# Kernel optimization log

Measured on AMD Instinct MI355X. Metric: run time of the kernel, lower is better.

The kernel has to match this reference:

```python
import jax, jax.numpy as jnp
import numpy as np

EPS_LN = 1e-5
EPS_ATTN = 1e-8
NUM_ITER = 3

B, N, DIN = 64, 4096, 256
K, D, H = 8, 256, 512


def layer_norm(x, g, b):
    m = jnp.mean(x, axis=-1, keepdims=True)
    v = jnp.mean((x - m) ** 2, axis=-1, keepdims=True)
    return (x - m) * jax.lax.rsqrt(v + EPS_LN) * g + b


def gru_cell(x, h, W_ih, b_ih, W_hh, b_hh):
    # torch GRUCell: gates ordered (reset, update, new)
    gi = x @ W_ih.T + b_ih  # [BK, 3D]
    gh = h @ W_hh.T + b_hh
    ir, iz, inn = jnp.split(gi, 3, axis=-1)
    hr, hz, hn = jnp.split(gh, 3, axis=-1)
    r = jax.nn.sigmoid(ir + hr)
    z = jax.nn.sigmoid(iz + hz)
    n = jnp.tanh(inn + r * hn)
    return (1.0 - z) * n + z * h


def setup_inputs() -> dict:
    key = jax.random.key(0)
    ks = jax.random.split(key, 16)
    s = 1.0 / np.sqrt(D)
    si = 1.0 / np.sqrt(DIN)
    inp = {
        'inputs': jax.random.normal(ks[0], (B, N, DIN), jnp.float32),
        'noise': jax.random.normal(ks[1], (B, K, D), jnp.float32),
        'slot_mu': jax.random.normal(ks[2], (1, 1, D), jnp.float32),
        'slot_log_sigma': jnp.zeros((1, 1, D), jnp.float32),
        'Wq': jax.random.uniform(ks[3], (D, D), jnp.float32, -s, s),
        'bq': jnp.zeros((D,), jnp.float32),
        'Wk': jax.random.uniform(ks[4], (D, DIN), jnp.float32, -si, si),
        'bk': jnp.zeros((D,), jnp.float32),
        'Wv': jax.random.uniform(ks[5], (D, DIN), jnp.float32, -si, si),
        'bv': jnp.zeros((D,), jnp.float32),
        'W_ih': jax.random.uniform(ks[6], (3 * D, D), jnp.float32, -s, s),
        'b_ih': jnp.zeros((3 * D,), jnp.float32),
        'W_hh': jax.random.uniform(ks[7], (3 * D, D), jnp.float32, -s, s),
        'b_hh': jnp.zeros((3 * D,), jnp.float32),
        'ln_in_g': jnp.ones((DIN,), jnp.float32), 'ln_in_b': jnp.zeros((DIN,), jnp.float32),
        'ln_s_g': jnp.ones((D,), jnp.float32), 'ln_s_b': jnp.zeros((D,), jnp.float32),
        'ln_ff_g': jnp.ones((D,), jnp.float32), 'ln_ff_b': jnp.zeros((D,), jnp.float32),
        'W1': jax.random.uniform(ks[8], (H, D), jnp.float32, -s, s),
        'b1': jnp.zeros((H,), jnp.float32),
        'W2': jax.random.uniform(ks[9], (D, H), jnp.float32, -1.0 / np.sqrt(H), 1.0 / np.sqrt(H)),
        'b2': jnp.zeros((D,), jnp.float32),
    }
    return inp


def reference(inputs, noise, slot_mu, slot_log_sigma, Wq, bq, Wk, bk, Wv, bv,
              W_ih, b_ih, W_hh, b_hh, ln_in_g, ln_in_b, ln_s_g, ln_s_b,
              ln_ff_g, ln_ff_b, W1, b1, W2, b2):
    scale = D ** -0.5
    slots = slot_mu + jnp.exp(slot_log_sigma) * noise  # [B,K,D]
    x = layer_norm(inputs, ln_in_g, ln_in_b)
    k = x @ Wk.T + bk  # [B,N,D]
    v = x @ Wv.T + bv  # [B,N,D]
    attn = None
    for _ in range(NUM_ITER):
        slots_prev = slots
        sn = layer_norm(slots, ln_s_g, ln_s_b)
        q = sn @ Wq.T + bq  # [B,K,D]
        dots = jnp.einsum('bkd,bnd->bkn', q, k) * scale
        attn = jax.nn.softmax(dots, axis=1)  # softmax over slots
        attn_norm = attn / (jnp.sum(attn, axis=-1, keepdims=True) + EPS_ATTN)
        updates = jnp.einsum('bkn,bnd->bkd', attn_norm, v)
        h = gru_cell(updates.reshape(-1, D), slots_prev.reshape(-1, D),
                     W_ih, b_ih, W_hh, b_hh).reshape(slots.shape)
        ff = layer_norm(h, ln_ff_g, ln_ff_b)
        slots = h + (jax.nn.relu(ff @ W1.T + b1) @ W2.T + b2)
    return slots, attn
```

## Files before the change

### kernel.cpp

```cpp
#include <hip/hip_runtime.h>
#include <hip/hip_bf16.h>
#include <math.h>

typedef __bf16 bf16x8 __attribute__((ext_vector_type(8)));
typedef float f32x4 __attribute__((ext_vector_type(4)));

#define DEV static __device__ __forceinline__

DEV unsigned short f2b(float f){
  unsigned int u = __float_as_uint(f);
  u += 0x7fffu + ((u>>16)&1u);
  return (unsigned short)(u>>16);
}
DEV float b2f(unsigned short h){ return __uint_as_float(((unsigned int)h)<<16); }
DEV unsigned int pck(float a, float b){
  return (unsigned int)f2b(a) | ((unsigned int)f2b(b)<<16);
}
DEV f32x4 mfma16(bf16x8 a, bf16x8 b, f32x4 c){
  return __builtin_amdgcn_mfma_f32_16x16x32_bf16(a,b,c,0,0,0);
}
DEV float sigm(float x){ return 1.f/(1.f+expf(-x)); }

__global__ __launch_bounds__(256) void k_slots_init(
    const float* __restrict__ noise, const float* __restrict__ mu,
    const float* __restrict__ ls, float* __restrict__ sf,
    unsigned short* __restrict__ sb){
  int i = blockIdx.x*256 + threadIdx.x;
  int d = i & 255;
  float val = mu[d] + expf(ls[d]) * noise[i];
  sf[i] = val; sb[i] = f2b(val);
}

__global__ __launch_bounds__(256) void k_prep_b16(
    const float* __restrict__ Whh, const float* __restrict__ W1,
    const float* __restrict__ W2,
    unsigned short* __restrict__ Whhb, unsigned short* __restrict__ W1b,
    unsigned short* __restrict__ W2b){
  int i = blockIdx.x*256 + threadIdx.x;
  if (i < 196608) Whhb[i] = f2b(Whh[i]);
  else if (i < 327680) W1b[i-196608] = f2b(W1[i-196608]);
  else if (i < 458752) W2b[i-327680] = f2b(W2[i-327680]);
}

__global__ __launch_bounds__(256) void k_pre1(
    const float* __restrict__ Wq, const float* __restrict__ Wk,
    const float* __restrict__ bq, const float* __restrict__ bk,
    unsigned short* __restrict__ WcT, float* __restrict__ bc,
    float* __restrict__ wqbk, float* __restrict__ cbk){
  int c = blockIdx.x, d = threadIdx.x;
  float acc = 0.f;
  for (int e=0;e<256;e++)
    acc += Wq[e*256+d] * Wk[e*256+c];
  WcT[c*256+d] = f2b(acc);
  __shared__ float red[256];
  red[d] = bq[d] * Wk[d*256+c];
  __syncthreads();
  for (int s2=128;s2>0;s2>>=1){ if (d<s2) red[d]+=red[d+s2]; __syncthreads(); }
  if (d==0) bc[c] = red[0];
  if (blockIdx.x==0){
    float a2=0.f;
    for (int e=0;e<256;e++) a2 += Wq[e*256+d]*bk[e];
    wqbk[d] = a2;
    __syncthreads();
    red[d] = bq[d]*bk[d];
    __syncthreads();
    for (int s2=128;s2>0;s2>>=1){ if (d<s2) red[d]+=red[d+s2]; __syncthreads(); }
    if (d==0) cbk[0] = red[0];
  }
}

__global__ __launch_bounds__(256) void k_pre2(
    const float* __restrict__ W_ih, const float* __restrict__ Wv,
    const float* __restrict__ bv, const float* __restrict__ b_ih,
    unsigned short* __restrict__ WvihT, float* __restrict__ bvih){
  int j = blockIdx.x, c = threadIdx.x;
  float acc=0.f;
  for (int d=0; d<256; d++)
    acc += W_ih[j*256+d] * Wv[d*256+c];
  WvihT[j*256+c] = f2b(acc);
  __shared__ float red[256];
  red[c] = bv[c] * W_ih[j*256+c];
  __syncthreads();
  for (int s2=128;s2>0;s2>>=1){ if (c<s2) red[c]+=red[c+s2]; __syncthreads(); }
  if (c==0) bvih[j] = red[0] + b_ih[j];
}

__global__ __launch_bounds__(256) void k_slot_q(
    const float* __restrict__ sf, const float* __restrict__ g,
    const float* __restrict__ be,
    const unsigned short* __restrict__ WcT, const float* __restrict__ bc,
    const float* __restrict__ wqbk, const float* __restrict__ cbk,
    unsigned short* __restrict__ qp, float* __restrict__ dotbias,
    float* __restrict__ attn_sum){
  __shared__ __align__(16) unsigned short sn[16][264];
  int b = blockIdx.x, t = threadIdx.x;
  if (t < 8) attn_sum[b*8+t] = 0.f;
  if (t < 8) dotbias[b*16+8+t] = 0.f;
  int r = t>>5, j = t&31;
  const float* pr = sf + (b*8+r)*256 + j*8;
  float v[8]; float s=0.f;
  #pragma unroll
  for (int i=0;i<8;i++){ v[i]=pr[i]; s+=v[i]; }
  s += __shfl_xor(s,1); s+=__shfl_xor(s,2); s+=__shfl_xor(s,4);
  s += __shfl_xor(s,8); s+=__shfl_xor(s,16);
  float m = s*(1.f/256.f);
  float vs=0.f;
  #pragma unroll
  for (int i=0;i<8;i++){ float d = v[i]-m; vs += d*d; }
  vs += __shfl_xor(vs,1); vs+=__shfl_xor(vs,2); vs+=__shfl_xor(vs,4);
  vs += __shfl_xor(vs,8); vs+=__shfl_xor(vs,16);
  float rstd = rsqrtf(vs*(1.f/256.f) + 1e-5f);
  float dp = 0.f;
  #pragma unroll
  for (int i=0;i<8;i++){
    int d = j*8+i;
    float snv = (v[i]-m)*rstd*g[d] + be[d];
    sn[r][d] = f2b(snv);
    dp += snv * wqbk[d];
  }
  dp += __shfl_xor(dp,1); dp+=__shfl_xor(dp,2); dp+=__shfl_xor(dp,4);
  dp += __shfl_xor(dp,8); dp+=__shfl_xor(dp,16);
  if (j==0) dotbias[b*16+r] = dp + cbk[0];
  for (int rr=8; rr<16; ++rr){ sn[rr][t]=0; if (t<8) sn[rr][256+t]=0; }
  __syncthreads();
  int lane = t&63, wv = t>>6, l16 = lane&15, quad = lane>>4;
  #pragma unroll
  for (int nt=0; nt<4; ++nt){
    int col = (wv*4+nt)*16 + l16;
    f32x4 acc = {0.f,0.f,0.f,0.f};
    #pragma unroll
    for (int kk=0;kk<8;kk++){
      int kd = kk*32 + quad*8;
      bf16x8 a = *(const bf16x8*)&sn[l16][kd];
      bf16x8 bb = *(const bf16x8*)(WcT + col*256 + kd);
      acc = mfma16(a,bb,acc);
    }
    float bcv = bc[col];
    #pragma unroll
    for (int ri=0;ri<4;ri++){
      int rw = quad*4+ri;
      qp[(b*16+rw)*256 + col] = f2b(acc[ri] + bcv);
    }
  }
}

__global__ __launch_bounds__(256) void k_iter(
    const float* __restrict__ in, const float* __restrict__ g,
    const float* __restrict__ be, const unsigned short* __restrict__ qp,
    const float* __restrict__ dotbias, float* __restrict__ attn_sum,
    float* __restrict__ upart, float* __restrict__ attn_out,
    const unsigned short* __restrict__ xc_r, unsigned short* __restrict__ xc_w){
  __shared__ __align__(16) unsigned short xt[64][264];
  __shared__ __align__(16) float al[64][8];
  __shared__ float bsum[8];
  int t = threadIdx.x;
  int b = blockIdx.x >> 3, sp = blockIdx.x & 7;
  if (t<8) bsum[t]=0.f;
  int lane=t&63, wv=t>>6, l16=lane&15, quad=lane>>4;
  bf16x8 aq[8];
  #pragma unroll
  for (int kk=0;kk<8;kk++)
    aq[kk] = *(const bf16x8*)(qp + ((size_t)(b*16+l16))*256 + kk*32+quad*8);
  float db[4];
  #pragma unroll
  for (int ri=0;ri<4;ri++) db[ri] = dotbias[b*16 + quad*4 + ri];
  float acc8[8] = {0.f,0.f,0.f,0.f,0.f,0.f,0.f,0.f};
  int rl = t>>3, j = t&7;
  for (int tile=0; tile<8; ++tile){
    int n0 = sp*512 + tile*64;
    __syncthreads();
    if (xc_r){
      #pragma unroll
      for (int p=0;p<2;p++){
        int row = p*32 + rl;
        const unsigned short* pr = xc_r + ((size_t)(b*4096 + n0 + row))*256 + j*32;
        #pragma unroll
        for (int c=0;c<4;c++)
          *(uint4*)&xt[row][j*32 + c*8] = *(const uint4*)(pr + c*8);
      }
    } else {
      #pragma unroll
      for (int p=0;p<2;p++){
        int row = p*32 + rl;
        const float* pr = in + ((size_t)(b*4096 + n0 + row))*256 + j*32;
        float v[32]; float s=0.f;
        #pragma unroll
        for (int c=0;c<8;c++) *(float4*)(v+c*4) = *(const float4*)(pr + c*4);
        #pragma unroll
        for (int i=0;i<32;i++) s += v[i];
        s += __shfl_xor(s,1); s+=__shfl_xor(s,2); s+=__shfl_xor(s,4);
        float m = s*(1.f/256.f);
        float vs=0.f;
        #pragma unroll
        for (int i=0;i<32;i++){ float d=v[i]-m; vs+=d*d; }
        vs+=__shfl_xor(vs,1); vs+=__shfl_xor(vs,2); vs+=__shfl_xor(vs,4);
        float rstd = rsqrtf(vs*(1.f/256.f)+1e-5f);
        #pragma unroll
        for (int c=0;c<4;c++){
          float o[8];
          #pragma unroll
          for (int q=0;q<8;q++){
            int d = j*32 + c*8 + q;
            o[q] = (v[c*8+q]-m)*rstd*g[d] + be[d];
          }
          uint4 w4;
          w4.x=pck(o[0],o[1]); w4.y=pck(o[2],o[3]);
          w4.z=pck(o[4],o[5]); w4.w=pck(o[6],o[7]);
          *(uint4*)&xt[row][j*32 + c*8] = w4;
          if (xc_w)
            *(uint4*)(xc_w + ((size_t)(b*4096 + n0 + row))*256 + j*32 + c*8) = w4;
        }
      }
    }
    __syncthreads();
    f32x4 acc = {0.f,0.f,0.f,0.f};
    #pragma unroll
    for (int kk=0;kk<8;kk++){
      int kd = kk*32 + quad*8;
      bf16x8 bb = *(const bf16x8*)&xt[wv*16 + l16][kd];
      acc = mfma16(aq[kk],bb,acc);
    }
    const float scale = 0.0625f;
    float val[4];
    #pragma unroll
    for (int ri=0;ri<4;ri++) val[ri] = (acc[ri] + db[ri]) * scale;
    float mx = fmaxf(fmaxf(val[0],val[1]), fmaxf(val[2],val[3]));
    mx = fmaxf(mx, __shfl_xor(mx,16));
    float e[4], s4=0.f;
    #pragma unroll
    for (int ri=0;ri<4;ri++){ e[ri] = expf(val[ri]-mx); s4 += e[ri]; }
    float s8 = s4 + __shfl_xor(s4,16);
    float inv = 1.f/s8;
    if (quad < 2){
      int nl = wv*16 + l16;
      #pragma unroll
      for (int ri=0;ri<4;ri++){
        float av = e[ri]*inv;
        int kr = quad*4+ri;
        al[nl][kr] = av;
        if (attn_out)
          attn_out[((size_t)(b*8+kr))*4096 + n0 + nl] = av;
        float ss = av;
        ss += __shfl_xor(ss,1); ss+=__shfl_xor(ss,2);
        ss += __shfl_xor(ss,4); ss+=__shfl_xor(ss,8);
        if (l16==0) atomicAdd(&bsum[kr], ss);
      }
    }
    __syncthreads();
    int c = t;
    for (int n=0;n<64;++n){
      float xv = b2f(xt[n][c]);
      float4 a0 = *(const float4*)&al[n][0];
      float4 a1 = *(const float4*)&al[n][4];
      acc8[0]+=a0.x*xv; acc8[1]+=a0.y*xv; acc8[2]+=a0.z*xv; acc8[3]+=a0.w*xv;
      acc8[4]+=a1.x*xv; acc8[5]+=a1.y*xv; acc8[6]+=a1.z*xv; acc8[7]+=a1.w*xv;
    }
  }
  float* o = upart + (size_t)sp*131072 + ((size_t)b*8)*256 + t;
  #pragma unroll
  for (int k2=0;k2<8;k2++) o[(size_t)k2*256] = acc8[k2];
  if (t<8) atomicAdd(&attn_sum[b*8+t], bsum[t]);
}

__global__ __launch_bounds__(256) void k_step(
    const float* __restrict__ upart, float* __restrict__ asum,
    float* __restrict__ sf, unsigned short* __restrict__ sb,
    const unsigned short* __restrict__ WvihT, const float* __restrict__ bvih,
    const unsigned short* __restrict__ Whhb, const float* __restrict__ bhh,
    const float* __restrict__ lnffg, const float* __restrict__ lnffb,
    const unsigned short* __restrict__ W1b, const float* __restrict__ b1,
    const unsigned short* __restrict__ W2b, const float* __restrict__ b2v,
    const float* __restrict__ lnsg, const float* __restrict__ lnsb,
    const unsigned short* __restrict__ WcT, const float* __restrict__ bc,
    const float* __restrict__ wqbk, const float* __restrict__ cbk,
    unsigned short* __restrict__ qp, float* __restrict__ dotb,
    float* __restrict__ out_slots, int last){
  __shared__ __align__(16) unsigned short ub16[16][264];
  __shared__ __align__(16) float hls[16][268];
  __shared__ __align__(16) unsigned short sn[16][264];
  __shared__ __align__(16) unsigned short s1t[16][520];
  __shared__ float redh[4][16], redq[4][16], mr[16], rs[16];
  int t = threadIdx.x;
  int Bk = blockIdx.x;
  int bb0 = Bk*2;
  int lane=t&63, wv=t>>6, l16=lane&15, quad=lane>>4;
  {
    int r16 = t>>4, c0 = (t&15)*16;
    size_t base = ((size_t)(Bk*16 + r16))*256 + c0;
    float4 a0={0,0,0,0}, a1={0,0,0,0}, a2={0,0,0,0}, a3={0,0,0,0};
    #pragma unroll
    for (int sp2=0; sp2<8; ++sp2){
      const float* p = upart + (size_t)sp2*131072 + base;
      float4 u0=*(const float4*)(p+0), u1=*(const float4*)(p+4),
             u2=*(const float4*)(p+8), u3=*(const float4*)(p+12);
      a0.x+=u0.x;a0.y+=u0.y;a0.z+=u0.z;a0.w+=u0.w;
      a1.x+=u1.x;a1.y+=u1.y;a1.z+=u1.z;a1.w+=u1.w;
      a2.x+=u2.x;a2.y+=u2.y;a2.z+=u2.z;a2.w+=u2.w;
      a3.x+=u3.x;a3.y+=u3.y;a3.z+=u3.z;a3.w+=u3.w;
    }
    float inv = 1.f/(asum[Bk*16 + r16] + 1e-8f);
    float uu[16] = {a0.x,a0.y,a0.z,a0.w,a1.x,a1.y,a1.z,a1.w,
                    a2.x,a2.y,a2.z,a2.w,a3.x,a3.y,a3.z,a3.w};
    #pragma unroll
    for (int c=0;c<16;c+=2){
      *(unsigned int*)&ub16[r16][c0+c] = pck(uu[c]*inv, uu[c+1]*inv);
    }
  }
  __syncthreads();
  if (t < 16) asum[Bk*16 + t] = 0.f;
  bf16x8 afi[8], afh[8];
  #pragma unroll
  for (int kk=0;kk<8;kk++){
    int kd = kk*32+quad*8;
    afi[kk] = *(const bf16x8*)&ub16[l16][kd];
    afh[kk] = *(const bf16x8*)(sb + ((size_t)(Bk*16+l16))*256 + kd);
  }
  float sh[4]={0,0,0,0}, sq[4]={0,0,0,0};
  #pragma unroll
  for (int jj=0;jj<4;jj++){
    int jt = wv*4 + jj;
    int dR = jt*16 + l16;
    f32x4 cIR={0,0,0,0}, cIZ={0,0,0,0}, cIN={0,0,0,0};
    f32x4 cHR={0,0,0,0}, cHZ={0,0,0,0}, cHN={0,0,0,0};
    #pragma unroll
    for (int kk=0;kk<8;kk++){
      int kd = kk*32+quad*8;
      cIR = mfma16(afi[kk], *(const bf16x8*)(WvihT + (size_t)dR*256 + kd), cIR);
      cIZ = mfma16(afi[kk], *(const bf16x8*)(WvihT + (size_t)(256+dR)*256 + kd), cIZ);
      cIN = mfma16(afi[kk], *(const bf16x8*)(WvihT + (size_t)(512+dR)*256 + kd), cIN);
      cHR = mfma16(afh[kk], *(const bf16x8*)(Whhb + (size_t)dR*256 + kd), cHR);
      cHZ = mfma16(afh[kk], *(const bf16x8*)(Whhb + (size_t)(256+dR)*256 + kd), cHZ);
      cHN = mfma16(afh[kk], *(const bf16x8*)(Whhb + (size_t)(512+dR)*256 + kd), cHN);
    }
    float biR = bvih[dR], biZ = bvih[256+dR], biN = bvih[512+dR];
    float bhR = bhh[dR], bhZ = bhh[256+dR], bhN = bhh[512+dR];
    #pragma unroll
    for (int ri=0;ri<4;ri++){
      int row = quad*4+ri;
      float hp = sf[((size_t)(Bk*16+row))*256 + dR];
      float rg = sigm(cIR[ri]+biR + cHR[ri]+bhR);
      float z  = sigm(cIZ[ri]+biZ + cHZ[ri]+bhZ);
      float nn = tanhf(cIN[ri]+biN + rg*(cHN[ri]+bhN));
      float h = (1.f-z)*nn + z*hp;
      hls[row][dR] = h;
      sh[ri] += h; sq[ri] += h*h;
    }
  }
  #pragma unroll
  for (int ri=0;ri<4;ri++){
    sh[ri]+=__shfl_xor(sh[ri],1); sh[ri]+=__shfl_xor(sh[ri],2);
    sh[ri]+=__shfl_xor(sh[ri],4); sh[ri]+=__shfl_xor(sh[ri],8);
    sq[ri]+=__shfl_xor(sq[ri],1); sq[ri]+=__shfl_xor(sq[ri],2);
    sq[ri]+=__shfl_xor(sq[ri],4); sq[ri]+=__shfl_xor(sq[ri],8);
  }
  if (l16==0){
    #pragma unroll
    for (int ri=0;ri<4;ri++){
      redh[wv][quad*4+ri] = sh[ri];
      redq[wv][quad*4+ri] = sq[ri];
    }
  }
  __syncthreads();
  if (t < 16){
    float s = redh[0][t]+redh[1][t]+redh[2][t]+redh[3][t];
    float q = redq[0][t]+redq[1][t]+redq[2][t]+redq[3][t];
    float m = s*(1.f/256.f);
    float var = q*(1.f/256.f) - m*m;
    mr[t] = m; rs[t] = rsqrtf(var + 1e-5f);
  }
  __syncthreads();
  {
    int row = t>>4, c0 = (t&15)*16;
    float m = mr[row], rstd = rs[row];
    #pragma unroll
    for (int c=0;c<16;c+=2){
      int d = c0+c;
      float o0 = (hls[row][d]-m)*rstd*lnffg[d] + lnffb[d];
      float o1 = (hls[row][d+1]-m)*rstd*lnffg[d+1] + lnffb[d+1];
      *(unsigned int*)&sn[row][d] = pck(o0,o1);
    }
  }
  __syncthreads();
  {
    bf16x8 af[8];
    #pragma unroll
    for (int kk=0;kk<8;kk++)
      af[kk] = *(const bf16x8*)&sn[l16][kk*32+quad*8];
    #pragma unroll
    for (int ct=wv*8; ct<wv*8+8; ++ct){
      int col = ct*16+l16;
      f32x4 acc={0,0,0,0};
      #pragma unroll
      for (int kk=0;kk<8;kk++)
        acc = mfma16(af[kk], *(const bf16x8*)(W1b + (size_t)col*256 + kk*32+quad*8), acc);
      float bb = b1[col];
      #pragma unroll
      for (int ri=0;ri<4;ri++){
        float v2 = acc[ri]+bb; v2 = v2>0.f? v2:0.f;
        s1t[quad*4+ri][col] = f2b(v2);
      }
    }
  }
  __syncthreads();
  {
    bf16x8 af[16];
    #pragma unroll
    for (int kk=0;kk<16;kk++)
      af[kk] = *(const bf16x8*)&s1t[l16][kk*32+quad*8];
    #pragma unroll
    for (int ct=wv*4; ct<wv*4+4; ++ct){
      int col = ct*16+l16;
      f32x4 acc={0,0,0,0};
      #pragma unroll
      for (int kk=0;kk<16;kk++)
        acc = mfma16(af[kk], *(const bf16x8*)(W2b + (size_t)col*512 + kk*32+quad*8), acc);
      float bb = b2v[col];
      #pragma unroll
      for (int ri=0;ri<4;ri++){
        int row = quad*4+ri;
        float v2 = acc[ri] + bb + hls[row][col];
        size_t gidx = ((size_t)(Bk*16+row))*256 + col;
        sf[gidx] = v2;
        sb[gidx] = f2b(v2);
        if (last) out_slots[gidx] = v2;
        hls[row][col] = v2;
      }
    }
  }
  if (!last){
    __syncthreads();
    {
      int row = t>>4, c0 = (t&15)*16;
      float ps=0.f, pq=0.f;
      float hv[16];
      #pragma unroll
      for (int c=0;c<16;c++){ hv[c]=hls[row][c0+c]; ps+=hv[c]; pq+=hv[c]*hv[c]; }
      ps+=__shfl_xor(ps,1); ps+=__shfl_xor(ps,2); ps+=__shfl_xor(ps,4); ps+=__shfl_xor(ps,8);
      pq+=__shfl_xor(pq,1); pq+=__shfl_xor(pq,2); pq+=__shfl_xor(pq,4); pq+=__shfl_xor(pq,8);
      float m = ps*(1.f/256.f);
      float var = pq*(1.f/256.f) - m*m;
      float rstd = rsqrtf(var + 1e-5f);
      float dp = 0.f;
      #pragma unroll
      for (int c=0;c<16;c+=2){
        int d = c0+c;
        float o0 = (hv[c]-m)*rstd*lnsg[d] + lnsb[d];
        float o1 = (hv[c+1]-m)*rstd*lnsg[d+1] + lnsb[d+1];
        dp += o0*wqbk[d] + o1*wqbk[d+1];
        *(unsigned int*)&sn[row][d] = pck(o0,o1);
      }
      dp+=__shfl_xor(dp,1); dp+=__shfl_xor(dp,2); dp+=__shfl_xor(dp,4); dp+=__shfl_xor(dp,8);
      if ((t&15)==0){
        int bloc = row>>3, rr = row&7;
        dotb[(bb0+bloc)*16 + rr] = dp + cbk[0];
      }
    }
    __syncthreads();
    {
      bf16x8 af[8];
      #pragma unroll
      for (int kk=0;kk<8;kk++)
        af[kk] = *(const bf16x8*)&sn[l16][kk*32+quad*8];
      #pragma unroll
      for (int ct=wv*4; ct<wv*4+4; ++ct){
        int col = ct*16+l16;
        f32x4 acc={0,0,0,0};
        #pragma unroll
        for (int kk=0;kk<8;kk++)
          acc = mfma16(af[kk], *(const bf16x8*)(WcT + (size_t)col*256 + kk*32+quad*8), acc);
        float bcv = bc[col];
        #pragma unroll
        for (int ri=0;ri<4;ri++){
          int row = quad*4+ri;
          int bloc = row>>3, rr = row&7;
          qp[((size_t)((bb0+bloc)*16 + rr))*256 + col] = f2b(acc[ri] + bcv);
        }
      }
    }
  }
}

extern "C" void kernel_launch(void* const* d_in, const int* in_sizes, int n_in,
                              void* d_out, int out_size, void* d_ws, size_t ws_size,
                              hipStream_t stream){
  const float* inputs  = (const float*)d_in[0];
  const float* noise   = (const float*)d_in[1];
  const float* slot_mu = (const float*)d_in[2];
  const float* slot_ls = (const float*)d_in[3];
  const float* Wq   = (const float*)d_in[4];
  const float* bq   = (const float*)d_in[5];
  const float* Wk   = (const float*)d_in[6];
  const float* bk   = (const float*)d_in[7];
  const float* Wv   = (const float*)d_in[8];
  const float* bv   = (const float*)d_in[9];
  const float* W_ih = (const float*)d_in[10];
  const float* b_ih = (const float*)d_in[11];
  const float* W_hh = (const float*)d_in[12];
  const float* b_hh = (const float*)d_in[13];
  const float* ln_in_g = (const float*)d_in[14];
  const float* ln_in_b = (const float*)d_in[15];
  const float* ln_s_g  = (const float*)d_in[16];
  const float* ln_s_b  = (const float*)d_in[17];
  const float* ln_ff_g = (const float*)d_in[18];
  const float* ln_ff_b = (const float*)d_in[19];
  const float* W1 = (const float*)d_in[20];
  const float* b1 = (const float*)d_in[21];
  const float* W2 = (const float*)d_in[22];
  const float* b2 = (const float*)d_in[23];

  char* w = (char*)d_ws;
  auto alloc = [&](size_t n)->char*{ char* p=w; w += (n+255)&~(size_t)255; return p; };
  unsigned short* xc   = (unsigned short*)alloc(134217728);
  float* upart         = (float*)alloc(4194304);
  unsigned short* qp   = (unsigned short*)alloc(524288);
  float* sf            = (float*)alloc(524288);
  unsigned short* sb   = (unsigned short*)alloc(262144);
  unsigned short* WcT  = (unsigned short*)alloc(131072);
  unsigned short* WvihT= (unsigned short*)alloc(393216);
  unsigned short* Whhb = (unsigned short*)alloc(393216);
  unsigned short* W1b  = (unsigned short*)alloc(262144);
  unsigned short* W2b  = (unsigned short*)alloc(262144);
  float* bc    = (float*)alloc(1024);
  float* wqbk  = (float*)alloc(1024);
  float* cbk   = (float*)alloc(256);
  float* bvih  = (float*)alloc(3072);
  float* dotb  = (float*)alloc(4096);
  float* asum  = (float*)alloc(2048);

  float* out_slots = (float*)d_out;
  float* out_attn  = out_slots + 131072;

  k_slots_init<<<dim3(512),dim3(256),0,stream>>>(noise, slot_mu, slot_ls, sf, sb);
  k_pre1<<<dim3(256),dim3(256),0,stream>>>(Wq, Wk, bq, bk, WcT, bc, wqbk, cbk);
  k_pre2<<<dim3(768),dim3(256),0,stream>>>(W_ih, Wv, bv, b_ih, WvihT, bvih);
  k_prep_b16<<<dim3(1792),dim3(256),0,stream>>>(W_hh, W1, W2, Whhb, W1b, W2b);
  k_slot_q<<<dim3(64),dim3(256),0,stream>>>(sf, ln_s_g, ln_s_b, WcT, bc, wqbk, cbk,
                                            qp, dotb, asum);

  for (int it=0; it<3; ++it){
    int last = (it==2);
    k_iter<<<dim3(512),dim3(256),0,stream>>>(
        inputs, ln_in_g, ln_in_b, qp, dotb, asum, upart,
        last ? out_attn : (float*)nullptr,
        it ? xc : (const unsigned short*)nullptr,
        it==0 ? xc : (unsigned short*)nullptr);
    k_step<<<dim3(32),dim3(256),0,stream>>>(
        upart, asum, sf, sb, WvihT, bvih, Whhb, b_hh,
        ln_ff_g, ln_ff_b, W1b, b1, W2b, b2,
        ln_s_g, ln_s_b, WcT, bc, wqbk, cbk,
        qp, dotb, last ? out_slots : (float*)nullptr, last);
  }
}
```

Before: 851.0 us.

## Split input layernorm into own kernel, prefetch tiles, double grid splits

Moves the input layernorm and bf16 conversion out of the first attention iteration into a standalone k_ln kernel, so all three k_iter passes just stream the cached bf16 activations. k_iter now splits each batch's sequence across 16 blocks instead of 8, and prefetches the next 64-row tile into registers while the current tile is being computed. It also sets launch bounds to 4 blocks per CU and unrolls the update accumulation loop. k_step runs one batch per block over 64 blocks, zero-padding the MFMA rows to 16. The aim is more parallelism and latency hiding, at the cost of an extra kernel launch, a separate full pass to write the normalized input, twice as many partial sums to reduce, and half-empty MFMA tiles in k_step.

```diff
diff --git a/kernel.cpp b/kernel.cpp
--- a/kernel.cpp
+++ b/kernel.cpp
@@ -83,6 +83,41 @@
   __syncthreads();
   for (int s2=128;s2>0;s2>>=1){ if (c<s2) red[c]+=red[c+s2]; __syncthreads(); }
   if (c==0) bvih[j] = red[0] + b_ih[j];
+}
+
+__global__ __launch_bounds__(256) void k_ln(
+    const float* __restrict__ in, const float* __restrict__ g,
+    const float* __restrict__ be, unsigned short* __restrict__ xc){
+  int t = threadIdx.x;
+  int row = blockIdx.x*32 + (t>>3);
+  int j = t&7;
+  const float* pr = in + (size_t)row*256 + j*32;
+  float v[32]; float s=0.f;
+  #pragma unroll
+  for (int c=0;c<8;c++) *(float4*)(v+c*4) = *(const float4*)(pr + c*4);
+  #pragma unroll
+  for (int i=0;i<32;i++) s += v[i];
+  s += __shfl_xor(s,1); s+=__shfl_xor(s,2); s+=__shfl_xor(s,4);
+  float m = s*(1.f/256.f);
+  float vs=0.f;
+  #pragma unroll
+  for (int i=0;i<32;i++){ float d=v[i]-m; vs+=d*d; }
+  vs+=__shfl_xor(vs,1); vs+=__shfl_xor(vs,2); vs+=__shfl_xor(vs,4);
+  float rstd = rsqrtf(vs*(1.f/256.f)+1e-5f);
+  unsigned short* po = xc + (size_t)row*256 + j*32;
+  #pragma unroll
+  for (int c=0;c<4;c++){
+    float o[8];
+    #pragma unroll
+    for (int q=0;q<8;q++){
+      int d = j*32 + c*8 + q;
+      o[q] = (v[c*8+q]-m)*rstd*g[d] + be[d];
+    }
+    uint4 w4;
+    w4.x=pck(o[0],o[1]); w4.y=pck(o[2],o[3]);
+    w4.z=pck(o[4],o[5]); w4.w=pck(o[6],o[7]);
+    *(uint4*)(po + c*8) = w4;
+  }
 }
 
 __global__ __launch_bounds__(256) void k_slot_q(
@@ -144,17 +179,16 @@
   }
 }
 
-__global__ __launch_bounds__(256) void k_iter(
-    const float* __restrict__ in, const float* __restrict__ g,
-    const float* __restrict__ be, const unsigned short* __restrict__ qp,
+__global__ __launch_bounds__(256,4) void k_iter(
+    const unsigned short* __restrict__ xc,
+    const unsigned short* __restrict__ qp,
     const float* __restrict__ dotbias, float* __restrict__ attn_sum,
-    float* __restrict__ upart, float* __restrict__ attn_out,
-    const unsigned short* __restrict__ xc_r, unsigned short* __restrict__ xc_w){
+    float* __restrict__ upart, float* __restrict__ attn_out){
   __shared__ __align__(16) unsigned short xt[64][264];
   __shared__ __align__(16) float al[64][8];
   __shared__ float bsum[8];
   int t = threadIdx.x;
-  int b = blockIdx.x >> 3, sp = blockIdx.x & 7;
+  int b = blockIdx.x >> 4, sp = blockIdx.x & 15;
   if (t<8) bsum[t]=0.f;
   int lane=t&63, wv=t>>6, l16=lane&15, quad=lane>>4;
   bf16x8 aq[8];
@@ -166,53 +200,32 @@
   for (int ri=0;ri<4;ri++) db[ri] = dotbias[b*16 + quad*4 + ri];
   float acc8[8] = {0.f,0.f,0.f,0.f,0.f,0.f,0.f,0.f};
   int rl = t>>3, j = t&7;
-  for (int tile=0; tile<8; ++tile){
-    int n0 = sp*512 + tile*64;
-    __syncthreads();
-    if (xc_r){
+  const unsigned short* cbase = xc + ((size_t)(b*4096 + sp*256))*256;
+  uint4 R[8];
+  #pragma unroll
+  for (int p=0;p<2;p++){
+    const unsigned short* pr = cbase + (size_t)(p*32+rl)*256 + j*32;
+    #pragma unroll
+    for (int c=0;c<4;c++) R[p*4+c] = *(const uint4*)(pr + c*8);
+  }
+  for (int tile=0; tile<4; ++tile){
+    #pragma unroll
+    for (int p=0;p<2;p++){
+      #pragma unroll
+      for (int c=0;c<4;c++)
+        *(uint4*)&xt[p*32+rl][j*32 + c*8] = R[p*4+c];
+    }
+    __syncthreads();
+    if (tile<3){
+      const unsigned short* nb = cbase + (size_t)(tile+1)*64*256;
       #pragma unroll
       for (int p=0;p<2;p++){
-        int row = p*32 + rl;
-        const unsigned short* pr = xc_r + ((size_t)(b*4096 + n0 + row))*256 + j*32;
+        const unsigned short* pr = nb + (size_t)(p*32+rl)*256 + j*32;
         #pragma unroll
-        for (int c=0;c<4;c++)
-          *(uint4*)&xt[row][j*32 + c*8] = *(const uint4*)(pr + c*8);
+        for (int c=0;c<4;c++) R[p*4+c] = *(const uint4*)(pr + c*8);
       }
-    } else {
-      #pragma unroll
-      for (int p=0;p<2;p++){
-        int row = p*32 + rl;
-        const float* pr = in + ((size_t)(b*4096 + n0 + row))*256 + j*32;
-        float v[32]; float s=0.f;
-        #pragma unroll
-        for (int c=0;c<8;c++) *(float4*)(v+c*4) = *(const float4*)(pr + c*4);
-        #pragma unroll
-        for (int i=0;i<32;i++) s += v[i];
-        s += __shfl_xor(s,1); s+=__shfl_xor(s,2); s+=__shfl_xor(s,4);
-        float m = s*(1.f/256.f);
-        float vs=0.f;
-        #pragma unroll
-        for (int i=0;i<32;i++){ float d=v[i]-m; vs+=d*d; }
-        vs+=__shfl_xor(vs,1); vs+=__shfl_xor(vs,2); vs+=__shfl_xor(vs,4);
-        float rstd = rsqrtf(vs*(1.f/256.f)+1e-5f);
-        #pragma unroll
-        for (int c=0;c<4;c++){
-          float o[8];
-          #pragma unroll
-          for (int q=0;q<8;q++){
-            int d = j*32 + c*8 + q;
-            o[q] = (v[c*8+q]-m)*rstd*g[d] + be[d];
-          }
-          uint4 w4;
-          w4.x=pck(o[0],o[1]); w4.y=pck(o[2],o[3]);
-          w4.z=pck(o[4],o[5]); w4.w=pck(o[6],o[7]);
-          *(uint4*)&xt[row][j*32 + c*8] = w4;
-          if (xc_w)
-            *(uint4*)(xc_w + ((size_t)(b*4096 + n0 + row))*256 + j*32 + c*8) = w4;
-        }
-      }
-    }
-    __syncthreads();
+    }
+    int n0 = sp*256 + tile*64;
     f32x4 acc = {0.f,0.f,0.f,0.f};
     #pragma unroll
     for (int kk=0;kk<8;kk++){
@@ -248,6 +261,7 @@
     }
     __syncthreads();
     int c = t;
+    #pragma unroll
     for (int n=0;n<64;++n){
       float xv = b2f(xt[n][c]);
       float4 a0 = *(const float4*)&al[n][0];
@@ -255,6 +269,7 @@
       acc8[0]+=a0.x*xv; acc8[1]+=a0.y*xv; acc8[2]+=a0.z*xv; acc8[3]+=a0.w*xv;
       acc8[4]+=a1.x*xv; acc8[5]+=a1.y*xv; acc8[6]+=a1.z*xv; acc8[7]+=a1.w*xv;
     }
+    __syncthreads();
   }
   float* o = upart + (size_t)sp*131072 + ((size_t)b*8)*256 + t;
   #pragma unroll
@@ -281,39 +296,37 @@
   __shared__ __align__(16) unsigned short s1t[16][520];
   __shared__ float redh[4][16], redq[4][16], mr[16], rs[16];
   int t = threadIdx.x;
-  int Bk = blockIdx.x;
-  int bb0 = Bk*2;
+  int b = blockIdx.x;
   int lane=t&63, wv=t>>6, l16=lane&15, quad=lane>>4;
   {
-    int r16 = t>>4, c0 = (t&15)*16;
-    size_t base = ((size_t)(Bk*16 + r16))*256 + c0;
-    float4 a0={0,0,0,0}, a1={0,0,0,0}, a2={0,0,0,0}, a3={0,0,0,0};
-    #pragma unroll
-    for (int sp2=0; sp2<8; ++sp2){
+    int r8 = t>>5, c0 = (t&31)*8;
+    size_t base = ((size_t)(b*8 + r8))*256 + c0;
+    float4 a0={0,0,0,0}, a1={0,0,0,0};
+    #pragma unroll
+    for (int sp2=0; sp2<16; ++sp2){
       const float* p = upart + (size_t)sp2*131072 + base;
-      float4 u0=*(const float4*)(p+0), u1=*(const float4*)(p+4),
-             u2=*(const float4*)(p+8), u3=*(const float4*)(p+12);
+      float4 u0=*(const float4*)(p+0), u1=*(const float4*)(p+4);
       a0.x+=u0.x;a0.y+=u0.y;a0.z+=u0.z;a0.w+=u0.w;
       a1.x+=u1.x;a1.y+=u1.y;a1.z+=u1.z;a1.w+=u1.w;
-      a2.x+=u2.x;a2.y+=u2.y;a2.z+=u2.z;a2.w+=u2.w;
-      a3.x+=u3.x;a3.y+=u3.y;a3.z+=u3.z;a3.w+=u3.w;
-    }
-    float inv = 1.f/(asum[Bk*16 + r16] + 1e-8f);
-    float uu[16] = {a0.x,a0.y,a0.z,a0.w,a1.x,a1.y,a1.z,a1.w,
-                    a2.x,a2.y,a2.z,a2.w,a3.x,a3.y,a3.z,a3.w};
-    #pragma unroll
-    for (int c=0;c<16;c+=2){
-      *(unsigned int*)&ub16[r16][c0+c] = pck(uu[c]*inv, uu[c+1]*inv);
-    }
-  }
-  __syncthreads();
-  if (t < 16) asum[Bk*16 + t] = 0.f;
+    }
+    float inv = 1.f/(asum[b*8 + r8] + 1e-8f);
+    float uu[8] = {a0.x,a0.y,a0.z,a0.w,a1.x,a1.y,a1.z,a1.w};
+    #pragma unroll
+    for (int c=0;c<8;c+=2)
+      *(unsigned int*)&ub16[r8][c0+c] = pck(uu[c]*inv, uu[c+1]*inv);
+    uint4 z = {0,0,0,0};
+    *(uint4*)&ub16[8+r8][c0] = z;
+  }
+  __syncthreads();
+  if (t < 8) asum[b*8 + t] = 0.f;
+  uint4 zz = {0,0,0,0};
+  bf16x8 z8 = *(bf16x8*)&zz;
   bf16x8 afi[8], afh[8];
   #pragma unroll
   for (int kk=0;kk<8;kk++){
     int kd = kk*32+quad*8;
     afi[kk] = *(const bf16x8*)&ub16[l16][kd];
-    afh[kk] = *(const bf16x8*)(sb + ((size_t)(Bk*16+l16))*256 + kd);
+    afh[kk] = (l16<8) ? *(const bf16x8*)(sb + ((size_t)(b*8+l16))*256 + kd) : z8;
   }
   float sh[4]={0,0,0,0}, sq[4]={0,0,0,0};
   #pragma unroll
@@ -337,7 +350,7 @@
     #pragma unroll
     for (int ri=0;ri<4;ri++){
       int row = quad*4+ri;
-      float hp = sf[((size_t)(Bk*16+row))*256 + dR];
+      float hp = (row<8) ? sf[((size_t)(b*8+row))*256 + dR] : 0.f;
       float rg = sigm(cIR[ri]+biR + cHR[ri]+bhR);
       float z  = sigm(cIZ[ri]+biZ + cHZ[ri]+bhZ);
       float nn = tanhf(cIN[ri]+biN + rg*(cHN[ri]+bhN));
@@ -419,11 +432,13 @@
       for (int ri=0;ri<4;ri++){
         int row = quad*4+ri;
         float v2 = acc[ri] + bb + hls[row][col];
-        size_t gidx = ((size_t)(Bk*16+row))*256 + col;
-        sf[gidx] = v2;
-        sb[gidx] = f2b(v2);
-        if (last) out_slots[gidx] = v2;
         hls[row][col] = v2;
+        if (row < 8){
+          size_t gidx = ((size_t)(b*8+row))*256 + col;
+          sf[gidx] = v2;
+          sb[gidx] = f2b(v2);
+          if (last) out_slots[gidx] = v2;
+        }
       }
     }
   }
@@ -450,10 +465,8 @@
         *(unsigned int*)&sn[row][d] = pck(o0,o1);
       }
       dp+=__shfl_xor(dp,1); dp+=__shfl_xor(dp,2); dp+=__shfl_xor(dp,4); dp+=__shfl_xor(dp,8);
-      if ((t&15)==0){
-        int bloc = row>>3, rr = row&7;
-        dotb[(bb0+bloc)*16 + rr] = dp + cbk[0];
-      }
+      if ((t&15)==0 && row<8)
+        dotb[b*16 + row] = dp + cbk[0];
     }
     __syncthreads();
     {
@@ -472,8 +485,8 @@
         #pragma unroll
         for (int ri=0;ri<4;ri++){
           int row = quad*4+ri;
-          int bloc = row>>3, rr = row&7;
-          qp[((size_t)((bb0+bloc)*16 + rr))*256 + col] = f2b(acc[ri] + bcv);
+          if (row < 8)
+            qp[((size_t)(b*16+row))*256 + col] = f2b(acc[ri] + bcv);
         }
       }
     }
@@ -511,7 +524,7 @@
   char* w = (char*)d_ws;
   auto alloc = [&](size_t n)->char*{ char* p=w; w += (n+255)&~(size_t)255; return p; };
   unsigned short* xc   = (unsigned short*)alloc(134217728);
-  float* upart         = (float*)alloc(4194304);
+  float* upart         = (float*)alloc(8388608);
   unsigned short* qp   = (unsigned short*)alloc(524288);
   float* sf            = (float*)alloc(524288);
   unsigned short* sb   = (unsigned short*)alloc(262144);
@@ -534,17 +547,16 @@
   k_pre1<<<dim3(256),dim3(256),0,stream>>>(Wq, Wk, bq, bk, WcT, bc, wqbk, cbk);
   k_pre2<<<dim3(768),dim3(256),0,stream>>>(W_ih, Wv, bv, b_ih, WvihT, bvih);
   k_prep_b16<<<dim3(1792),dim3(256),0,stream>>>(W_hh, W1, W2, Whhb, W1b, W2b);
+  k_ln<<<dim3(8192),dim3(256),0,stream>>>(inputs, ln_in_g, ln_in_b, xc);
   k_slot_q<<<dim3(64),dim3(256),0,stream>>>(sf, ln_s_g, ln_s_b, WcT, bc, wqbk, cbk,
                                             qp, dotb, asum);
 
   for (int it=0; it<3; ++it){
     int last = (it==2);
-    k_iter<<<dim3(512),dim3(256),0,stream>>>(
-        inputs, ln_in_g, ln_in_b, qp, dotb, asum, upart,
-        last ? out_attn : (float*)nullptr,
-        it ? xc : (const unsigned short*)nullptr,
-        it==0 ? xc : (unsigned short*)nullptr);
-    k_step<<<dim3(32),dim3(256),0,stream>>>(
+    k_iter<<<dim3(1024),dim3(256),0,stream>>>(
+        xc, qp, dotb, asum, upart,
+        last ? out_attn : (float*)nullptr);
+    k_step<<<dim3(64),dim3(256),0,stream>>>(
         upart, asum, sf, sb, WvihT, bvih, Whhb, b_hh,
         ln_ff_g, ln_ff_b, W1b, b1, W2b, b2,
         ln_s_g, ln_s_b, WcT, bc, wqbk, cbk,
```

Measured after the change: 952.9 us. 1.12x slower.
